# Kernel optimization log

Measured on AMD Instinct MI355X. Metric: run time of the kernel, lower is better.

The kernel has to match this reference:

```python
import jax, jax.numpy as jnp
import numpy as np
from jax import lax

MODES = 16
DEPTH = 8
NPH = 8  # photons = sum(init_state); init_state = [1]*8 + [0]*8
IDX = np.arange(NPH)  # output_indices derived from init_state
PI = np.pi
CHUNK = 4096  # pairs per permanent chunk (memory control, mirrors chunk_subsets idea)


def setup_inputs() -> dict:
    key = jax.random.key(0)
    k1, k2, k3 = jax.random.split(key, 3)
    x = jax.random.normal(k1, (256, 64), dtype=jnp.float32)
    W = jax.random.normal(k2, (120, 64), dtype=jnp.float32) / np.sqrt(64.0)
    b = jax.random.normal(k3, (120,), dtype=jnp.float32) * 0.01
    return {"x": x, "W": W, "b": b}


def _forward(x, W, b):
    N = x.shape[0]
    # fc1 + sigmoid embedding -> angle pairs
    x_emb = jax.nn.sigmoid(x @ W.T + b)              # (N, 120)
    tbu = x_emb.reshape(N, -1, 2)                    # (N, T, 2)
    theta = tbu[:, :, 0] * (PI / 2)
    phi = tbu[:, :, 1] * (2 * PI)
    ct = jnp.cos(theta).astype(jnp.complex64)
    st = jnp.sin(theta).astype(jnp.complex64)
    ep = jnp.exp(1j * phi.astype(jnp.complex64))
    # 2x2 tunable beam-splitter unitaries: [[e^{i phi} c, -s], [e^{i phi} s, c]]
    row0 = jnp.stack([ep * ct, -st], axis=-1)
    row1 = jnp.stack([ep * st, ct], axis=-1)
    blocks = jnp.stack([row0, row1], axis=-2)        # (N, T, 2, 2)

    # Apply block-diagonal layers. Block-diag matmul only mixes row pairs,
    # so update row segments directly instead of building (modes,modes) UBS.
    U = jnp.broadcast_to(jnp.eye(MODES, dtype=jnp.complex64), (N, MODES, MODES))
    nb_even, nb_odd = MODES // 2, (MODES - 2) // 2
    n_before = 0
    for d in range(DEPTH):
        if d % 2 == 0:
            nb, off = nb_even, 0
        else:
            nb, off = nb_odd, 1
        blk = blocks[:, n_before:n_before + nb]                      # (N, nb, 2, 2)
        seg = U[:, off:off + 2 * nb, :].reshape(N, nb, 2, MODES)     # row pairs
        new = jnp.einsum('nkab,nkbm->nkam', blk, seg).reshape(N, 2 * nb, MODES)
        U = U.at[:, off:off + 2 * nb, :].set(new)
        n_before += nb

    # Photonic Gram: K[a,b] = |perm( (U_a^dag U_b)[idx, idx] )|^2.
    # Only the idx-columns of U enter: V = U[:, :, idx], submatrix = V_a^dag V_b.
    V = U[:, :, IDX]                                  # (N, MODES, n)
    G = jnp.einsum('ami,bmj->abij', V.conj(), V)      # (N, N, n, n)

    n = NPH
    subsets = jnp.arange(1, 1 << n)                   # (S,), S = 2^n - 1
    masks = (subsets[:, None] >> jnp.arange(n)[None, :]) & 1   # (S, n)
    signs = (1 - 2 * ((n - masks.sum(axis=1)) & 1)).astype(jnp.complex64)
    maskc = masks.astype(jnp.complex64)

    A = G.reshape(N * N, n, n)
    nc = (N * N) // CHUNK

    def perm_chunk(Ac):  # Ryser: sum_S (-1)^{n-|S|} prod_i sum_{j in S} A_ij
        ss = jnp.einsum('cij,sj->csi', Ac, maskc)     # (c, S, n) subset row-sums
        pr = jnp.prod(ss, axis=2)                     # (c, S)
        return jnp.sum(pr * signs, axis=1)            # (c,)

    perms = lax.map(perm_chunk, A.reshape(nc, CHUNK, n, n)).reshape(N * N)
    K = (jnp.abs(perms) ** 2).astype(jnp.float32).reshape(N, N)
    di = jnp.arange(N)
    K = K.at[di, di].set(1.0)
    return x_emb, K


def reference(x, W, b):
    return _forward(x, W, b)
```

## Files before the change

### kernel.cpp

```cpp
#include <hip/hip_runtime.h>
#include <math.h>

#define NS 256
#define EMB 120
#define NBLK 60
#define MODES 16
#define NPH 8

__device__ __forceinline__ float2 cmul(float2 a, float2 b) {
    float2 r;
    r.x = fmaf(a.x, b.x, -(a.y * b.y));
    r.y = fmaf(a.x, b.y,   a.y * b.x);
    return r;
}

__global__ __launch_bounds__(128) void emb_v_kernel(
    const float* __restrict__ x, const float* __restrict__ W,
    const float* __restrict__ bias, float* __restrict__ out_emb,
    float2* __restrict__ Vws)
{
    const int s = blockIdx.x;
    const int t = threadIdx.x;
    __shared__ float emb[EMB];
    __shared__ float ctA[NBLK], stA[NBLK], exA[NBLK], eyA[NBLK];

    if (t < EMB) {
        const float* xr = x + s * 64;
        const float* wr = W + t * 64;
        float acc = bias[t];
        #pragma unroll
        for (int k = 0; k < 64; ++k) acc = fmaf(xr[k], wr[k], acc);
        float e = 1.0f / (1.0f + expf(-acc));
        emb[t] = e;
        out_emb[s * EMB + t] = e;
    }
    __syncthreads();

    if (t < NBLK) {
        float th = emb[2 * t]     * 1.57079632679489662f;
        float ph = emb[2 * t + 1] * 6.28318530717958648f;
        float st, ct, sp, cp;
        sincosf(th, &st, &ct);
        sincosf(ph, &sp, &cp);
        ctA[t] = ct; stA[t] = st; exA[t] = cp; eyA[t] = sp;
    }
    __syncthreads();

    if (t < NPH) {
        const int c = t;
        float2 u[MODES];
        #pragma unroll
        for (int m = 0; m < MODES; ++m) {
            u[m].x = (m == c) ? 1.0f : 0.0f;
            u[m].y = 0.0f;
        }
        int bi = 0;
        #pragma unroll
        for (int d = 0; d < 8; ++d) {
            const int off = d & 1;
            const int nb = 8 - off;
            #pragma unroll
            for (int k = 0; k < nb; ++k) {
                float ct = ctA[bi], st = stA[bi], ex = exA[bi], ey = eyA[bi];
                ++bi;
                const int r0 = off + 2 * k;
                float2 u0 = u[r0], u1 = u[r0 + 1];
                float2 n0, n1;
                n0.x = ex * ct * u0.x - ey * ct * u0.y - st * u1.x;
                n0.y = ex * ct * u0.y + ey * ct * u0.x - st * u1.y;
                n1.x = ex * st * u0.x - ey * st * u0.y + ct * u1.x;
                n1.y = ex * st * u0.y + ey * st * u0.x + ct * u1.y;
                u[r0] = n0; u[r0 + 1] = n1;
            }
        }
        #pragma unroll
        for (int m = 0; m < MODES; ++m)
            Vws[(s * MODES + m) * NPH + c] = u[m];
    }
}

__global__ __launch_bounds__(256, 1) void perm_kernel(
    const float2* __restrict__ Vws, float* __restrict__ outK)
{
    __shared__ float2 lds_a[16][130];
    __shared__ float2 lds_b[16][130];

    const int tid = threadIdx.x;
    const int ta = blockIdx.x >> 4;
    const int tb = blockIdx.x & 15;

    const float4* srcA = (const float4*)(Vws + (size_t)ta * 16 * 128);
    const float4* srcB = (const float4*)(Vws + (size_t)tb * 16 * 128);
    #pragma unroll
    for (int q = 0; q < 4; ++q) {
        int idx = q * 256 + tid;
        int row = idx >> 6;
        int pos = (idx & 63) * 2;
        float4 fa = srcA[idx];
        float4 fb = srcB[idx];
        lds_a[row][pos].x     = fa.x; lds_a[row][pos].y     = fa.y;
        lds_a[row][pos + 1].x = fa.z; lds_a[row][pos + 1].y = fa.w;
        lds_b[row][pos].x     = fb.x; lds_b[row][pos].y     = fb.y;
        lds_b[row][pos + 1].x = fb.z; lds_b[row][pos + 1].y = fb.w;
    }
    __syncthreads();

    const int tx = tid & 15;
    const int ty = tid >> 4;

    float2 G[8][8];
    #pragma unroll
    for (int i = 0; i < 8; ++i)
        #pragma unroll
        for (int j = 0; j < 8; ++j) { G[i][j].x = 0.f; G[i][j].y = 0.f; }

    #pragma unroll 1
    for (int m = 0; m < 16; ++m) {
        float2 va[8], vb[8];
        #pragma unroll
        for (int i = 0; i < 8; ++i) va[i] = lds_a[ty][m * 8 + i];
        #pragma unroll
        for (int j = 0; j < 8; ++j) vb[j] = lds_b[tx][m * 8 + j];
        #pragma unroll
        for (int i = 0; i < 8; ++i)
            #pragma unroll
            for (int j = 0; j < 8; ++j) {
                G[i][j].x = fmaf(va[i].x, vb[j].x, fmaf(va[i].y, vb[j].y, G[i][j].x));
                G[i][j].y = fmaf(va[i].x, vb[j].y, fmaf(-va[i].y, vb[j].x, G[i][j].y));
            }
    }

    float2 rs[8];
    #pragma unroll
    for (int i = 0; i < 8; ++i) {
        float sx = 0.f, sy = 0.f;
        #pragma unroll
        for (int j = 0; j < 8; ++j) { sx += G[i][j].x; sy += G[i][j].y; }
        rs[i].x = sx; rs[i].y = sy;
    }

    float2 acc;

#define PRODTREE(OUT) do {                                            \
        float2 p01 = cmul(rs[0], rs[1]);                              \
        float2 p23 = cmul(rs[2], rs[3]);                              \
        float2 p45 = cmul(rs[4], rs[5]);                              \
        float2 p67 = cmul(rs[6], rs[7]);                              \
        float2 q0  = cmul(p01, p23);                                  \
        float2 q1  = cmul(p45, p67);                                  \
        OUT = cmul(q0, q1);                                           \
    } while (0)

#define UPD(J, S) do {                                                \
        _Pragma("unroll")                                             \
        for (int i = 0; i < 8; ++i) {                                 \
            rs[i].x = fmaf((S), G[i][J].x, rs[i].x);                  \
            rs[i].y = fmaf((S), G[i][J].y, rs[i].y);                  \
        }                                                             \
    } while (0)

#define TERM(TS) do {                                                 \
        float2 pr; PRODTREE(pr);                                      \
        acc.x = fmaf((TS), pr.x, acc.x);                              \
        acc.y = fmaf((TS), pr.y, acc.y);                              \
    } while (0)

    PRODTREE(acc);

    #pragma unroll 1
    for (int p = 0; p < 16; ++p) {
        const float s4 = (p & 1) ? 2.f : -2.f;
        UPD(1, -2.f); TERM(-1.f);
        UPD(2, -2.f); TERM( 1.f);
        UPD(1,  2.f); TERM(-1.f);
        UPD(3,  s4 ); TERM( 1.f);
        UPD(1, -2.f); TERM(-1.f);
        UPD(2,  2.f); TERM( 1.f);
        UPD(1,  2.f); TERM(-1.f);
        if (p < 15) {
            const int q = p + 1;
            const int c = __builtin_ctz(q);
            const float s = ((q >> (c + 1)) & 1) ? 2.f : -2.f;
            switch (c) {
                case 0: UPD(4, s); break;
                case 1: UPD(5, s); break;
                case 2: UPD(6, s); break;
                default: UPD(7, s); break;
            }
            TERM(1.f);
        }
    }
#undef UPD
#undef TERM
#undef PRODTREE

    const int a = ta * 16 + ty;
    const int b = tb * 16 + tx;
    float K = fmaf(acc.x, acc.x, acc.y * acc.y) * (1.0f / 16384.0f);
    if (a == b) K = 1.0f;
    outK[a * 256 + b] = K;
}

extern "C" void kernel_launch(void* const* d_in, const int* in_sizes, int n_in,
                              void* d_out, int out_size, void* d_ws, size_t ws_size,
                              hipStream_t stream) {
    const float* x    = (const float*)d_in[0];
    const float* W    = (const float*)d_in[1];
    const float* bias = (const float*)d_in[2];
    float* out     = (float*)d_out;
    float* out_emb = out;
    float* outK    = out + NS * EMB;
    float2* Vws    = (float2*)d_ws;

    emb_v_kernel<<<NS, 128, 0, stream>>>(x, W, bias, out_emb, Vws);
    perm_kernel<<<NS, 256, 0, stream>>>(Vws, outK);
}
```

Baseline: 80.89 us.

## Split each permanent across four threads via Gray-code subset partition

Each pair's Ryser permanent is now spread over four lanes. Each lane fixes the signs of columns 6 and 7 and walks the 32-step Gray code over the remaining columns, with the loop fully unrolled. Partial sums are combined with cross-lane shuffles. The Gram products are computed cooperatively (2 rows per thread) and exchanged through shared memory. The grid grows from 256 to 1024 blocks of 8x8 pairs, which raises parallelism on the device, at the cost of more LDS traffic, an extra barrier and duplicated Gram loading.

```diff
diff --git a/kernel.cpp b/kernel.cpp
--- a/kernel.cpp
+++ b/kernel.cpp
@@ -82,60 +82,88 @@
 __global__ __launch_bounds__(256, 1) void perm_kernel(
     const float2* __restrict__ Vws, float* __restrict__ outK)
 {
-    __shared__ float2 lds_a[16][130];
-    __shared__ float2 lds_b[16][130];
+    __shared__ float2 sva[8][132];
+    __shared__ float2 svb[8][132];
+    __shared__ float2 sG[64][66];
 
     const int tid = threadIdx.x;
-    const int ta = blockIdx.x >> 4;
-    const int tb = blockIdx.x & 15;
-
-    const float4* srcA = (const float4*)(Vws + (size_t)ta * 16 * 128);
-    const float4* srcB = (const float4*)(Vws + (size_t)tb * 16 * 128);
-    #pragma unroll
-    for (int q = 0; q < 4; ++q) {
-        int idx = q * 256 + tid;
+    const int ta = blockIdx.x >> 5;
+    const int tb = blockIdx.x & 31;
+
+    const float4* srcA = (const float4*)(Vws + (size_t)ta * 8 * 128);
+    const float4* srcB = (const float4*)(Vws + (size_t)tb * 8 * 128);
+    #pragma unroll
+    for (int r = 0; r < 2; ++r) {
+        int idx = r * 256 + tid;
         int row = idx >> 6;
-        int pos = (idx & 63) * 2;
-        float4 fa = srcA[idx];
-        float4 fb = srcB[idx];
-        lds_a[row][pos].x     = fa.x; lds_a[row][pos].y     = fa.y;
-        lds_a[row][pos + 1].x = fa.z; lds_a[row][pos + 1].y = fa.w;
-        lds_b[row][pos].x     = fb.x; lds_b[row][pos].y     = fb.y;
-        lds_b[row][pos + 1].x = fb.z; lds_b[row][pos + 1].y = fb.w;
-    }
-    __syncthreads();
-
-    const int tx = tid & 15;
-    const int ty = tid >> 4;
-
-    float2 G[8][8];
-    #pragma unroll
-    for (int i = 0; i < 8; ++i)
-        #pragma unroll
-        for (int j = 0; j < 8; ++j) { G[i][j].x = 0.f; G[i][j].y = 0.f; }
+        int c4  = idx & 63;
+        *(float4*)&sva[row][c4 * 2] = srcA[idx];
+        *(float4*)&svb[row][c4 * 2] = srcB[idx];
+    }
+    __syncthreads();
+
+    const int p  = tid >> 2;
+    const int q  = tid & 3;
+    const int pa = p >> 3;
+    const int pb = p & 7;
+
+    float2 Ga[2][8];
+    #pragma unroll
+    for (int i = 0; i < 2; ++i)
+        #pragma unroll
+        for (int j = 0; j < 8; ++j) { Ga[i][j].x = 0.f; Ga[i][j].y = 0.f; }
 
     #pragma unroll 1
     for (int m = 0; m < 16; ++m) {
-        float2 va[8], vb[8];
-        #pragma unroll
-        for (int i = 0; i < 8; ++i) va[i] = lds_a[ty][m * 8 + i];
-        #pragma unroll
-        for (int j = 0; j < 8; ++j) vb[j] = lds_b[tx][m * 8 + j];
-        #pragma unroll
-        for (int i = 0; i < 8; ++i)
-            #pragma unroll
-            for (int j = 0; j < 8; ++j) {
-                G[i][j].x = fmaf(va[i].x, vb[j].x, fmaf(va[i].y, vb[j].y, G[i][j].x));
-                G[i][j].y = fmaf(va[i].x, vb[j].y, fmaf(-va[i].y, vb[j].x, G[i][j].y));
-            }
-    }
+        float4 va4 = *(const float4*)&sva[pa][m * 8 + 2 * q];
+        float2 a0; a0.x = va4.x; a0.y = va4.y;
+        float2 a1; a1.x = va4.z; a1.y = va4.w;
+        float2 vb[8];
+        #pragma unroll
+        for (int jj = 0; jj < 4; ++jj) {
+            float4 b4 = *(const float4*)&svb[pb][m * 8 + 2 * jj];
+            vb[2 * jj].x     = b4.x; vb[2 * jj].y     = b4.y;
+            vb[2 * jj + 1].x = b4.z; vb[2 * jj + 1].y = b4.w;
+        }
+        #pragma unroll
+        for (int j = 0; j < 8; ++j) {
+            Ga[0][j].x = fmaf(a0.x, vb[j].x, fmaf(a0.y, vb[j].y, Ga[0][j].x));
+            Ga[0][j].y = fmaf(a0.x, vb[j].y, fmaf(-a0.y, vb[j].x, Ga[0][j].y));
+            Ga[1][j].x = fmaf(a1.x, vb[j].x, fmaf(a1.y, vb[j].y, Ga[1][j].x));
+            Ga[1][j].y = fmaf(a1.x, vb[j].y, fmaf(-a1.y, vb[j].x, Ga[1][j].y));
+        }
+    }
+    #pragma unroll
+    for (int i = 0; i < 2; ++i)
+        #pragma unroll
+        for (int jj = 0; jj < 4; ++jj) {
+            float4 w;
+            w.x = Ga[i][2 * jj].x;     w.y = Ga[i][2 * jj].y;
+            w.z = Ga[i][2 * jj + 1].x; w.w = Ga[i][2 * jj + 1].y;
+            *(float4*)&sG[p][(2 * q + i) * 8 + 2 * jj] = w;
+        }
+    __syncthreads();
+
+    float2 G[8][8];
+    #pragma unroll
+    for (int i = 0; i < 8; ++i)
+        #pragma unroll
+        for (int jj = 0; jj < 4; ++jj) {
+            float4 g4 = *(const float4*)&sG[p][i * 8 + 2 * jj];
+            G[i][2 * jj].x     = g4.x; G[i][2 * jj].y     = g4.y;
+            G[i][2 * jj + 1].x = g4.z; G[i][2 * jj + 1].y = g4.w;
+        }
+
+    const float d6 = (q & 1) ? -1.f : 1.f;
+    const float d7 = (q & 2) ? -1.f : 1.f;
 
     float2 rs[8];
     #pragma unroll
     for (int i = 0; i < 8; ++i) {
-        float sx = 0.f, sy = 0.f;
-        #pragma unroll
-        for (int j = 0; j < 8; ++j) { sx += G[i][j].x; sy += G[i][j].y; }
+        float sx = G[i][0].x + G[i][1].x + G[i][2].x + G[i][3].x + G[i][4].x + G[i][5].x;
+        float sy = G[i][0].y + G[i][1].y + G[i][2].y + G[i][3].y + G[i][4].y + G[i][5].y;
+        sx = fmaf(d6, G[i][6].x, sx); sx = fmaf(d7, G[i][7].x, sx);
+        sy = fmaf(d6, G[i][6].y, sy); sy = fmaf(d7, G[i][7].y, sy);
         rs[i].x = sx; rs[i].y = sy;
     }
 
@@ -166,39 +194,53 @@
     } while (0)
 
     PRODTREE(acc);
-
-    #pragma unroll 1
-    for (int p = 0; p < 16; ++p) {
-        const float s4 = (p & 1) ? 2.f : -2.f;
-        UPD(1, -2.f); TERM(-1.f);
-        UPD(2, -2.f); TERM( 1.f);
-        UPD(1,  2.f); TERM(-1.f);
-        UPD(3,  s4 ); TERM( 1.f);
-        UPD(1, -2.f); TERM(-1.f);
-        UPD(2,  2.f); TERM( 1.f);
-        UPD(1,  2.f); TERM(-1.f);
-        if (p < 15) {
-            const int q = p + 1;
-            const int c = __builtin_ctz(q);
-            const float s = ((q >> (c + 1)) & 1) ? 2.f : -2.f;
-            switch (c) {
-                case 0: UPD(4, s); break;
-                case 1: UPD(5, s); break;
-                case 2: UPD(6, s); break;
-                default: UPD(7, s); break;
-            }
-            TERM(1.f);
-        }
-    }
+    UPD(1, -2.f); TERM(-1.f);
+    UPD(2, -2.f); TERM( 1.f);
+    UPD(1,  2.f); TERM(-1.f);
+    UPD(3, -2.f); TERM( 1.f);
+    UPD(1, -2.f); TERM(-1.f);
+    UPD(2,  2.f); TERM( 1.f);
+    UPD(1,  2.f); TERM(-1.f);
+    UPD(4, -2.f); TERM( 1.f);
+    UPD(1, -2.f); TERM(-1.f);
+    UPD(2, -2.f); TERM( 1.f);
+    UPD(1,  2.f); TERM(-1.f);
+    UPD(3,  2.f); TERM( 1.f);
+    UPD(1, -2.f); TERM(-1.f);
+    UPD(2,  2.f); TERM( 1.f);
+    UPD(1,  2.f); TERM(-1.f);
+    UPD(5, -2.f); TERM( 1.f);
+    UPD(1, -2.f); TERM(-1.f);
+    UPD(2, -2.f); TERM( 1.f);
+    UPD(1,  2.f); TERM(-1.f);
+    UPD(3, -2.f); TERM( 1.f);
+    UPD(1, -2.f); TERM(-1.f);
+    UPD(2,  2.f); TERM( 1.f);
+    UPD(1,  2.f); TERM(-1.f);
+    UPD(4,  2.f); TERM( 1.f);
+    UPD(1, -2.f); TERM(-1.f);
+    UPD(2, -2.f); TERM( 1.f);
+    UPD(1,  2.f); TERM(-1.f);
+    UPD(3,  2.f); TERM( 1.f);
+    UPD(1, -2.f); TERM(-1.f);
+    UPD(2,  2.f); TERM( 1.f);
+    UPD(1,  2.f); TERM(-1.f);
 #undef UPD
 #undef TERM
 #undef PRODTREE
 
-    const int a = ta * 16 + ty;
-    const int b = tb * 16 + tx;
-    float K = fmaf(acc.x, acc.x, acc.y * acc.y) * (1.0f / 16384.0f);
-    if (a == b) K = 1.0f;
-    outK[a * 256 + b] = K;
+    const float sq = d6 * d7;
+    float ax = acc.x * sq, ay = acc.y * sq;
+    ax += __shfl_xor(ax, 1); ay += __shfl_xor(ay, 1);
+    ax += __shfl_xor(ax, 2); ay += __shfl_xor(ay, 2);
+
+    if (q == 0) {
+        const int a = ta * 8 + pa;
+        const int b = tb * 8 + pb;
+        float K = fmaf(ax, ax, ay * ay) * (1.0f / 16384.0f);
+        if (a == b) K = 1.0f;
+        outK[a * 256 + b] = K;
+    }
 }
 
 extern "C" void kernel_launch(void* const* d_in, const int* in_sizes, int n_in,
@@ -213,5 +255,5 @@
     float2* Vws    = (float2*)d_ws;
 
     emb_v_kernel<<<NS, 128, 0, stream>>>(x, W, bias, out_emb, Vws);
-    perm_kernel<<<NS, 256, 0, stream>>>(Vws, outK);
-}
+    perm_kernel<<<1024, 256, 0, stream>>>(Vws, outK);
+}
```

New measurement: 82.34 us. No clear change (+1.8%).
